# Optimization experiments

Measured on AMD Instinct MI355X. Metric: run time of the kernel, lower is better.

## Reference

```python
import jax, jax.numpy as jnp
import numpy as np

B, S, DIM, H, HD = 4, 1024, 1280, 16, 80
SCALE = HD ** -0.5
ROPE_THETA = 10000.0


def rotate_half(x):
    x1, x2 = jnp.split(x, 2, axis=-1)
    return jnp.concatenate([-x2, x1], axis=-1)


def setup_inputs() -> dict:
    key = jax.random.key(0)
    ks = jax.random.split(key, 5)
    x = jax.random.normal(ks[0], (B, S, DIM), dtype=jnp.float32)
    Wqkv = jax.random.normal(ks[1], (DIM, 3 * DIM), dtype=jnp.float32) * 0.02
    bqkv = jax.random.normal(ks[2], (3 * DIM,), dtype=jnp.float32) * 0.01
    Wproj = jax.random.normal(ks[3], (DIM, DIM), dtype=jnp.float32) * 0.02
    bproj = jax.random.normal(ks[4], (DIM,), dtype=jnp.float32) * 0.01
    # realistic rotary tables: (S, HD) with duplicated freq halves (matches rotate_half layout)
    inv_freq = 1.0 / (ROPE_THETA ** (jnp.arange(0, HD, 2, dtype=jnp.float32) / HD))
    freqs = jnp.outer(jnp.arange(S, dtype=jnp.float32), inv_freq)  # (S, HD/2)
    emb = jnp.concatenate([freqs, freqs], axis=-1)  # (S, HD)
    rope_cos = jnp.cos(emb)
    rope_sin = jnp.sin(emb)
    return {"x": x, "rope_cos": rope_cos, "rope_sin": rope_sin,
            "Wqkv": Wqkv, "bqkv": bqkv, "Wproj": Wproj, "bproj": bproj}


def reference(x, rope_cos, rope_sin, Wqkv, bqkv, Wproj, bproj):
    b, s, d = x.shape
    qkv = (x @ Wqkv + bqkv).reshape(b, s, 3, H, HD)
    q, k, v = qkv[:, :, 0], qkv[:, :, 1], qkv[:, :, 2]  # each (b, s, H, HD)
    cos = rope_cos[None, :, None, :]  # (1, s, 1, HD)
    sin = rope_sin[None, :, None, :]
    q = q * cos + rotate_half(q) * sin
    k = k * cos + rotate_half(k) * sin
    # SDPA with all-ones mask (full attention)
    scores = jnp.einsum("bqhd,bkhd->bhqk", q, k) * SCALE
    probs = jax.nn.softmax(scores, axis=-1)
    out = jnp.einsum("bhqk,bkhd->bqhd", probs, v).reshape(b, s, d)
    return out @ Wproj + bproj
```

## Files before the change

### kernel.cpp

```cpp
#include <hip/hip_runtime.h>
#include <math.h>

#define SCALE_F 0.11180339887498949f
#define HDP 96

typedef short  short8  __attribute__((ext_vector_type(8)));
typedef short  short4v __attribute__((ext_vector_type(4)));
typedef float  f32x4   __attribute__((ext_vector_type(4)));
typedef __bf16 bf16x8  __attribute__((ext_vector_type(8)));

__device__ __forceinline__ float bf2f(short s) {
  union { unsigned u; float f; } v;
  v.u = ((unsigned)(unsigned short)s) << 16;
  return v.f;
}
__device__ __forceinline__ short f2b(float f) {
  __bf16 h = (__bf16)f;
  return __builtin_bit_cast(short, h);
}
__device__ __forceinline__ bool probe_is_bf16(const unsigned* probe) {
  return (probe[1] & 0xFFFFu) != 0u;
}
__device__ __forceinline__ float load_scalar(const void* p, int i, bool isb) {
  return isb ? bf2f(((const short*)p)[i]) : ((const float*)p)[i];
}

__device__ __forceinline__ void gload_lds16(const short* g, short* l) {
  __builtin_amdgcn_global_load_lds(
      (const __attribute__((address_space(1))) void*)g,
      (__attribute__((address_space(3))) void*)l, 16, 0, 0);
}

template <typename V>
__device__ __forceinline__ auto mfma_try(V a, V b, f32x4 c, int)
    -> decltype(__builtin_amdgcn_mfma_f32_16x16x32_bf16(a, b, c, 0, 0, 0)) {
  return __builtin_amdgcn_mfma_f32_16x16x32_bf16(a, b, c, 0, 0, 0);
}
template <typename V>
__device__ __forceinline__ f32x4 mfma_try(V a, V b, f32x4 c, long) {
  return __builtin_amdgcn_mfma_f32_16x16x32_bf16(
      __builtin_bit_cast(bf16x8, a), __builtin_bit_cast(bf16x8, b), c, 0, 0, 0);
}
__device__ __forceinline__ f32x4 MFMA(short8 a, short8 b, f32x4 c) {
  return mfma_try(a, b, c, 0);
}

__global__ __launch_bounds__(256) void cvt_x_kernel(
    const void* __restrict__ xin, short* __restrict__ xout,
    const unsigned* __restrict__ probe) {
  bool isb = probe_is_bf16(probe);
  size_t i = ((size_t)blockIdx.x * 256 + threadIdx.x) * 8;
  if (isb) {
    *(short8*)&xout[i] = *(const short8*)((const short*)xin + i);
  } else {
    const float* f = (const float*)xin + i;
    float4 a0 = *(const float4*)f;
    float4 a1 = *(const float4*)(f + 4);
    short8 sv;
    sv[0] = f2b(a0.x); sv[1] = f2b(a0.y); sv[2] = f2b(a0.z); sv[3] = f2b(a0.w);
    sv[4] = f2b(a1.x); sv[5] = f2b(a1.y); sv[6] = f2b(a1.z); sv[7] = f2b(a1.w);
    *(short8*)&xout[i] = sv;
  }
}

__global__ __launch_bounds__(256) void transpose_kernel(
    const void* __restrict__ in, short* __restrict__ out, int R, int C,
    const unsigned* __restrict__ probe) {
  bool isb = probe_is_bf16(probe);
  __shared__ float tile[32][33];
  int t = threadIdx.x;
  int bx = blockIdx.x;
  int by = blockIdx.y;
  int r = t >> 3, c4 = (t & 7) * 4;
  size_t idx = (size_t)(by * 32 + r) * C + bx * 32 + c4;
  if (isb) {
    short4v v = *(const short4v*)((const short*)in + idx);
    tile[r][c4 + 0] = bf2f(v[0]);
    tile[r][c4 + 1] = bf2f(v[1]);
    tile[r][c4 + 2] = bf2f(v[2]);
    tile[r][c4 + 3] = bf2f(v[3]);
  } else {
    float4 v = *(const float4*)((const float*)in + idx);
    tile[r][c4 + 0] = v.x;
    tile[r][c4 + 1] = v.y;
    tile[r][c4 + 2] = v.z;
    tile[r][c4 + 3] = v.w;
  }
  __syncthreads();
  int rr = t >> 3, k4 = (t & 7) * 4;
  short4v o;
  o[0] = f2b(tile[k4 + 0][rr]);
  o[1] = f2b(tile[k4 + 1][rr]);
  o[2] = f2b(tile[k4 + 2][rr]);
  o[3] = f2b(tile[k4 + 3][rr]);
  *(short4v*)&out[(size_t)(bx * 32 + rr) * R + by * 32 + k4] = o;
}

__global__ __launch_bounds__(512, 2) void gemm_qkv_kernel(
    const short* __restrict__ X, const short* __restrict__ Wt,
    const void* __restrict__ bias, const unsigned* __restrict__ probe,
    short* __restrict__ Qw, short* __restrict__ Kw, short* __restrict__ Vt) {
  const int K = 1280;
  __shared__ short Al[2][2][8192];
  __shared__ short Bl[2][2][8192];
  int t = threadIdx.x;
  int bm = blockIdx.x / 15, bn = blockIdx.x % 15;
  int m0 = bm * 256, n0 = bn * 256;
  int w = t >> 6, lane = t & 63;
  int quad = lane >> 4, l16 = lane & 15, l8 = l16 & 7;
  int arow = (w >> 2) * 64 + l16;
  int brow = (w & 3) * 32 + l16;
  int sr = t >> 3, t8s = t * 8;
  int sjs = (t & 7) ^ (sr & 7);
  int soff0 = ((quad ^ l8) * 8);
  int soff1 = (((4 + quad) ^ l8) * 8);
  f32x4 acc[2][2][4][2] = {};

#define STAGE8(PTR, R0, KOFF, LP)                                            \
  {                                                                          \
    const short* g_ = (PTR) + (size_t)((R0) + sr) * 1280 + (KOFF) + sjs * 8; \
    gload_lds16(g_, (LP) + t8s);                                             \
    gload_lds16(g_ + 64 * 1280, (LP) + t8s + 4096);                          \
  }

#define PHASE(S, HA, HB, QM, QN, STAGE_CODE, DO_VW)                          \
  {                                                                          \
    short8 af[4][2], bfv[2][2];                                              \
    _Pragma("unroll") for (int mt = 0; mt < 4; mt++) {                       \
      int rp_ = (arow + mt * 16) * 64;                                       \
      af[mt][0] = *(const short8*)&Al[S][HA][rp_ + soff0];                   \
      af[mt][1] = *(const short8*)&Al[S][HA][rp_ + soff1];                   \
    }                                                                        \
    _Pragma("unroll") for (int nt = 0; nt < 2; nt++) {                       \
      int rp_ = (brow + nt * 16) * 64;                                       \
      bfv[nt][0] = *(const short8*)&Bl[S][HB][rp_ + soff0];                  \
      bfv[nt][1] = *(const short8*)&Bl[S][HB][rp_ + soff1];                  \
    }                                                                        \
    STAGE_CODE;                                                              \
    __builtin_amdgcn_s_barrier();                                            \
    asm volatile("s_waitcnt lgkmcnt(0)" ::: "memory");                       \
    __builtin_amdgcn_sched_barrier(0);                                       \
    __builtin_amdgcn_s_setprio(1);                                           \
    _Pragma("unroll") for (int mt = 0; mt < 4; mt++)                         \
      _Pragma("unroll") for (int nt = 0; nt < 2; nt++) {                     \
        acc[QM][QN][mt][nt] = MFMA(af[mt][0], bfv[nt][0], acc[QM][QN][mt][nt]); \
        acc[QM][QN][mt][nt] = MFMA(af[mt][1], bfv[nt][1], acc[QM][QN][mt][nt]); \
      }                                                                      \
    __builtin_amdgcn_s_setprio(0);                                           \
    if (DO_VW) {                                                             \
      asm volatile("s_waitcnt vmcnt(4)" ::: "memory");                       \
      __builtin_amdgcn_sched_barrier(0);                                     \
    }                                                                        \
    __builtin_amdgcn_s_barrier();                                            \
  }

  STAGE8(X,  m0,       0,  &Al[0][0][0]);
  STAGE8(X,  m0 + 128, 0,  &Al[0][1][0]);
  STAGE8(Wt, n0,       0,  &Bl[0][0][0]);
  STAGE8(Wt, n0 + 128, 0,  &Bl[0][1][0]);
  STAGE8(X,  m0,       64, &Al[1][0][0]);
  STAGE8(Wt, n0,       64, &Bl[1][0][0]);
  asm volatile("s_waitcnt vmcnt(4)" ::: "memory");
  __builtin_amdgcn_sched_barrier(0);
  __builtin_amdgcn_s_barrier();

  for (int i = 0; i < 10; i++) {
    int k1 = (2 * i + 1) * 64;
    int k2 = (2 * i + 2) * 64; if (k2 >= K) k2 = 0;
    int k3 = (2 * i + 3) * 64; if (k3 >= K) k3 = 0;
    PHASE(0, 0, 0, 0, 0, STAGE8(X,  m0 + 128, k1, &Al[1][1][0]), 0);
    PHASE(0, 0, 1, 0, 1, STAGE8(Wt, n0 + 128, k1, &Bl[1][1][0]), 0);
    PHASE(0, 1, 0, 1, 0, STAGE8(X,  m0,       k2, &Al[0][0][0]), 0);
    PHASE(0, 1, 1, 1, 1, STAGE8(Wt, n0,       k2, &Bl[0][0][0]), 1);
    PHASE(1, 0, 0, 0, 0, STAGE8(X,  m0 + 128, k2, &Al[0][1][0]), 0);
    PHASE(1, 0, 1, 0, 1, STAGE8(Wt, n0 + 128, k2, &Bl[0][1][0]), 0);
    PHASE(1, 1, 0, 1, 0, STAGE8(X,  m0,       k3, &Al[1][0][0]), 0);
    PHASE(1, 1, 1, 1, 1, STAGE8(Wt, n0,       k3, &Bl[1][0][0]), 1);
  }
  asm volatile("s_waitcnt vmcnt(0)" ::: "memory");
  __builtin_amdgcn_sched_barrier(0);

  bool isb = probe_is_bf16(probe);
  float bv[2][2];
#pragma unroll
  for (int qn = 0; qn < 2; qn++)
#pragma unroll
    for (int nt = 0; nt < 2; nt++)
      bv[qn][nt] =
          load_scalar(bias, n0 + qn * 128 + (w & 3) * 32 + nt * 16 + l16, isb);
#pragma unroll
  for (int qm = 0; qm < 2; qm++)
#pragma unroll
    for (int mt = 0; mt < 4; mt++) {
      int mbase = m0 + qm * 128 + (w >> 2) * 64 + mt * 16 + quad * 4;
      int b = mbase >> 10, sbase = mbase & 1023;
#pragma unroll
      for (int qn = 0; qn < 2; qn++)
#pragma unroll
        for (int nt = 0; nt < 2; nt++) {
          int n = n0 + qn * 128 + (w & 3) * 32 + nt * 16 + l16;
          int which = n / 1280;
          int rmod = n - which * 1280;
          int h = rmod / 80;
          int d = rmod - h * 80;
          int bh = b * 16 + h;
          if (which == 2) {
            short4v vv;
#pragma unroll
            for (int reg = 0; reg < 4; reg++)
              vv[reg] = f2b(acc[qm][qn][mt][nt][reg] + bv[qn][nt]);
            *(short4v*)&Vt[((size_t)bh * 80 + d) * 1024 + sbase] = vv;
          } else {
            short* dst = (which == 0 ? Qw : Kw);
#pragma unroll
            for (int reg = 0; reg < 4; reg++)
              dst[((size_t)bh * 1024 + sbase + reg) * HDP + d] =
                  f2b(acc[qm][qn][mt][nt][reg] + bv[qn][nt]);
          }
        }
    }
#undef PHASE
#undef STAGE8
}

__global__ __launch_bounds__(256) void rope_kernel(
    short* __restrict__ Qw, short* __restrict__ Kw,
    const void* __restrict__ cosb, const void* __restrict__ sinb,
    const unsigned* __restrict__ probe) {
  bool isb = probe_is_bf16(probe);
  int t = threadIdx.x;
  int w = t >> 6, lane = t & 63;
  int job = blockIdx.x * 4 + w;
  int which = job & 1;
  int row = job >> 1;
  int s = row & 1023;
  short* ptr = (which ? Kw : Qw) + (size_t)row * HDP;
  float scale = which ? 1.0f : SCALE_F;
  if (lane < 40) {
    float p0 = bf2f(ptr[lane]);
    float p1 = bf2f(ptr[lane + 40]);
    float c0 = load_scalar(cosb, s * 80 + lane, isb);
    float s0 = load_scalar(sinb, s * 80 + lane, isb);
    float c1 = load_scalar(cosb, s * 80 + lane + 40, isb);
    float s1 = load_scalar(sinb, s * 80 + lane + 40, isb);
    ptr[lane] = f2b((p0 * c0 - p1 * s0) * scale);
    ptr[lane + 40] = f2b((p1 * c1 + p0 * s1) * scale);
  } else if (lane < 56) {
    ptr[40 + lane] = 0;
  }
}

__global__ __launch_bounds__(512, 4) void attn_kernel(
    const short* __restrict__ Qw, const short* __restrict__ Kw,
    const short* __restrict__ Vt, short* __restrict__ out) {
  __shared__ short Klds[64 * 104];
  __shared__ short Vlds[80 * 72];
  __shared__ short Ps[8][16 * 72];
  int t = threadIdx.x;
  int w = t >> 6, lane = t & 63;
  int quad = lane >> 4, l16 = lane & 15;
  int bh = blockIdx.x & 63;
  int qt = blockIdx.x >> 6;
  int q0 = qt * 128;
  const short* Kb = Kw + (size_t)bh * 1024 * HDP;
  const short* Vb = Vt + (size_t)bh * 80 * 1024;

  short8 aq[3];
  {
    const short* qrow = Qw + ((size_t)bh * 1024 + q0 + w * 16 + l16) * HDP;
#pragma unroll
    for (int ks = 0; ks < 3; ks++)
      aq[ks] = *(const short8*)&qrow[ks * 32 + quad * 8];
  }

  short8 kreg[2], vreg[2];
#define PREFETCH(c)                                                        \
  {                                                                        \
    {                                                                      \
      int row = t / 12, col = (t % 12) * 8;                                \
      kreg[0] = *(const short8*)&Kb[(size_t)((c) + row) * HDP + col];      \
    }                                                                      \
    if (t < 256) {                                                         \
      int idx = 512 + t;                                                   \
      int row = idx / 12, col = (idx % 12) * 8;                            \
      kreg[1] = *(const short8*)&Kb[(size_t)((c) + row) * HDP + col];      \
    }                                                                      \
    {                                                                      \
      int d = t >> 3, s0 = (t & 7) * 8;                                    \
      vreg[0] = *(const short8*)&Vb[(size_t)d * 1024 + (c) + s0];          \
    }                                                                      \
    if (t < 128) {                                                         \
      int idx = 512 + t;                                                   \
      int d = idx >> 3, s0 = (idx & 7) * 8;                                \
      vreg[1] = *(const short8*)&Vb[(size_t)d * 1024 + (c) + s0];          \
    }                                                                      \
  }
#define STORE_LDS()                                                        \
  {                                                                        \
    {                                                                      \
      int row = t / 12, col = (t % 12) * 8;                                \
      *(short8*)&Klds[row * 104 + col] = kreg[0];                          \
    }                                                                      \
    if (t < 256) {                                                         \
      int idx = 512 + t;                                                   \
      int row = idx / 12, col = (idx % 12) * 8;                            \
      *(short8*)&Klds[row * 104 + col] = kreg[1];                          \
    }                                                                      \
    {                                                                      \
      int d = t >> 3, s0 = (t & 7) * 8;                                    \
      *(short8*)&Vlds[d * 72 + s0] = vreg[0];                              \
    }                                                                      \
    if (t < 128) {                                                         \
      int idx = 512 + t;                                                   \
      int d = idx >> 3, s0 = (idx & 7) * 8;                                \
      *(short8*)&Vlds[d * 72 + s0] = vreg[1];                              \
    }                                                                      \
  }

  PREFETCH(0);
  STORE_LDS();
  __syncthreads();

  f32x4 ofr[5] = {};
  float lsum[4] = {0.f, 0.f, 0.f, 0.f};
  short* Pw = &Ps[w][0];

  for (int c = 0; c < 1024; c += 64) {
    if (c + 64 < 1024) PREFETCH(c + 64);
    f32x4 sf[4] = {};
#pragma unroll
    for (int nt = 0; nt < 4; nt++) {
      short8 bk0 = *(const short8*)&Klds[(nt * 16 + l16) * 104 + 0 * 32 + quad * 8];
      short8 bk1 = *(const short8*)&Klds[(nt * 16 + l16) * 104 + 1 * 32 + quad * 8];
      short8 bk2 = *(const short8*)&Klds[(nt * 16 + l16) * 104 + 2 * 32 + quad * 8];
      sf[nt] = MFMA(aq[0], bk0, sf[nt]);
      sf[nt] = MFMA(aq[1], bk1, sf[nt]);
      sf[nt] = MFMA(aq[2], bk2, sf[nt]);
    }
#pragma unroll
    for (int r = 0; r < 4; r++) {
      float p0 = __expf(fminf(sf[0][r], 30.f));
      float p1 = __expf(fminf(sf[1][r], 30.f));
      float p2 = __expf(fminf(sf[2][r], 30.f));
      float p3 = __expf(fminf(sf[3][r], 30.f));
      sf[0][r] = p0; sf[1][r] = p1; sf[2][r] = p2; sf[3][r] = p3;
      lsum[r] += (p0 + p1) + (p2 + p3);
    }
#pragma unroll
    for (int nt = 0; nt < 4; nt++)
#pragma unroll
      for (int r = 0; r < 4; r++)
        Pw[(quad * 4 + r) * 72 + nt * 16 + l16] = f2b(sf[nt][r]);
    __threadfence_block();
    short8 ap[2];
#pragma unroll
    for (int ks = 0; ks < 2; ks++)
      ap[ks] = *(const short8*)&Pw[l16 * 72 + ks * 32 + quad * 8];
#pragma unroll
    for (int nt = 0; nt < 5; nt++) {
      short8 bv0 = *(const short8*)&Vlds[(nt * 16 + l16) * 72 + 0 * 32 + quad * 8];
      short8 bv1 = *(const short8*)&Vlds[(nt * 16 + l16) * 72 + 1 * 32 + quad * 8];
      ofr[nt] = MFMA(ap[0], bv0, ofr[nt]);
      ofr[nt] = MFMA(ap[1], bv1, ofr[nt]);
    }
    __syncthreads();
    if (c + 64 < 1024) {
      STORE_LDS();
      __syncthreads();
    }
  }
#pragma unroll
  for (int off = 1; off < 16; off <<= 1)
#pragma unroll
    for (int r = 0; r < 4; r++) lsum[r] += __shfl_xor(lsum[r], off);
  float inv[4];
#pragma unroll
  for (int r = 0; r < 4; r++) inv[r] = 1.f / lsum[r];
  int b = bh >> 4, h = bh & 15;
#pragma unroll
  for (int nt = 0; nt < 5; nt++) {
    int d = nt * 16 + l16;
#pragma unroll
    for (int r = 0; r < 4; r++) {
      int s = q0 + w * 16 + quad * 4 + r;
      out[((size_t)(b * 1024 + s)) * 1280 + h * 80 + d] = f2b(ofr[nt][r] * inv[r]);
    }
  }
}

__global__ __launch_bounds__(256) void gemm_proj_kernel(
    const short* __restrict__ A, const short* __restrict__ Wt,
    const void* __restrict__ bias, const unsigned* __restrict__ probe,
    float* __restrict__ out) {
  const int K = 1280;
  __shared__ short As[2][128 * 32];
  __shared__ short Bs[2][128 * 32];
  int t = threadIdx.x;
  int bm = blockIdx.x / 10;
  int bn = blockIdx.x % 10;
  int m0 = bm * 128, n0 = bn * 128;
  int w = t >> 6, lane = t & 63;
  int wm = w & 1, wn = w >> 1;
  int quad = lane >> 4, l16 = lane & 15;
  int row = t >> 2, ch = (t & 3) * 8, row2 = row + 64;
  int t8 = t * 8;
  const short* Ar  = A  + (size_t)(m0 + row)  * K + ch;
  const short* Ar2 = A  + (size_t)(m0 + row2) * K + ch;
  const short* Wr  = Wt + (size_t)(n0 + row)  * K + ch;
  const short* Wr2 = Wt + (size_t)(n0 + row2) * K + ch;
  f32x4 acc[4][4] = {};
  gload_lds16(Ar,  &As[0][t8]);
  gload_lds16(Ar2, &As[0][t8 + 2048]);
  gload_lds16(Wr,  &Bs[0][t8]);
  gload_lds16(Wr2, &Bs[0][t8 + 2048]);
  __syncthreads();
  int p = 0;
#define PROJ_COMPUTE(pp)                                                      \
  {                                                                           \
    short8 af[4], bfr[4];                                                     \
    _Pragma("unroll") for (int mt = 0; mt < 4; mt++)                          \
        af[mt] = *(const short8*)&As[pp][(wm * 64 + mt * 16 + l16) * 32 + quad * 8]; \
    _Pragma("unroll") for (int nt = 0; nt < 4; nt++)                          \
        bfr[nt] = *(const short8*)&Bs[pp][(wn * 64 + nt * 16 + l16) * 32 + quad * 8]; \
    _Pragma("unroll") for (int mt = 0; mt < 4; mt++)                          \
        _Pragma("unroll") for (int nt = 0; nt < 4; nt++)                      \
            acc[mt][nt] = MFMA(af[mt], bfr[nt], acc[mt][nt]);                 \
  }
  for (int k0 = 32; k0 < K; k0 += 32, p ^= 1) {
    gload_lds16(Ar + k0,  &As[p ^ 1][t8]);
    gload_lds16(Ar2 + k0, &As[p ^ 1][t8 + 2048]);
    gload_lds16(Wr + k0,  &Bs[p ^ 1][t8]);
    gload_lds16(Wr2 + k0, &Bs[p ^ 1][t8 + 2048]);
    PROJ_COMPUTE(p);
    __syncthreads();
  }
  PROJ_COMPUTE(p);
  bool isb = probe_is_bf16(probe);
  float bv[4];
#pragma unroll
  for (int nt = 0; nt < 4; nt++)
    bv[nt] = load_scalar(bias, n0 + wn * 64 + nt * 16 + l16, isb);
#pragma unroll
  for (int mt = 0; mt < 4; mt++) {
#pragma unroll
    for (int nt = 0; nt < 4; nt++) {
      int n = n0 + wn * 64 + nt * 16 + l16;
#pragma unroll
      for (int reg = 0; reg < 4; reg++) {
        int m = m0 + wm * 64 + mt * 16 + quad * 4 + reg;
        out[(size_t)m * 1280 + n] = acc[mt][nt][reg] + bv[nt];
      }
    }
  }
}

extern "C" void kernel_launch(void* const* d_in, const int* in_sizes, int n_in,
                              void* d_out, int out_size, void* d_ws, size_t ws_size,
                              hipStream_t stream) {
  const void* x        = d_in[0];
  const void* rope_cos = d_in[1];
  const void* rope_sin = d_in[2];
  const void* Wqkv     = d_in[3];
  const void* bqkv     = d_in[4];
  const void* Wproj    = d_in[5];
  const void* bproj    = d_in[6];
  const unsigned* probe = (const unsigned*)rope_cos;
  char* ws = (char*)d_ws;
  short* Wt1 = (short*)(ws + 0);
  short* Wt2 = (short*)(ws + 9830400);
  short* Qw  = (short*)(ws + 13107200);
  short* Kw  = (short*)(ws + 25690112);
  short* Vt  = (short*)(ws + 38273024);
  short* Xb  = (short*)(ws + 48758784);
  short* At  = (short*)(ws + 48758784);

  cvt_x_kernel<<<2560, 256, 0, stream>>>(x, Xb, probe);
  transpose_kernel<<<dim3(3840 / 32, 1280 / 32), 256, 0, stream>>>(Wqkv, Wt1, 1280, 3840, probe);
  transpose_kernel<<<dim3(1280 / 32, 1280 / 32), 256, 0, stream>>>(Wproj, Wt2, 1280, 1280, probe);
  gemm_qkv_kernel<<<240, 512, 0, stream>>>(Xb, Wt1, bqkv, probe, Qw, Kw, Vt);
  rope_kernel<<<32768, 256, 0, stream>>>(Qw, Kw, rope_cos, rope_sin, probe);
  attn_kernel<<<512, 512, 0, stream>>>(Qw, Kw, Vt, At);
  gemm_proj_kernel<<<32 * 10, 256, 0, stream>>>(At, Wt2, bproj, probe, (float*)d_out);
}
```

Measured before the change: 244.4 us.

## Double-buffer attention K/V tiles in LDS and drop redundant barriers

The attention kernel now keeps two LDS buffers for the K and V tiles, alternating between them each iteration. The next tile is stored into the buffer not being read, which removes one __syncthreads per key chunk. Separately, the GEMM phase macro drops the s_barrier that sat between staging and the MFMA block, leaving only the trailing barrier. The double buffer roughly doubles the K/V LDS footprint, which may lower how many attention blocks fit per CU. The removed GEMM barrier relies on the remaining barriers and waitcnts to keep LDS reads and writes correctly ordered.

```diff
diff --git a/kernel.cpp b/kernel.cpp
--- a/kernel.cpp
+++ b/kernel.cpp
@@ -137,7 +137,6 @@
       bfv[nt][1] = *(const short8*)&Bl[S][HB][rp_ + soff1];                  \
     }                                                                        \
     STAGE_CODE;                                                              \
-    __builtin_amdgcn_s_barrier();                                            \
     asm volatile("s_waitcnt lgkmcnt(0)" ::: "memory");                       \
     __builtin_amdgcn_sched_barrier(0);                                       \
     __builtin_amdgcn_s_setprio(1);                                           \
@@ -253,8 +252,8 @@
 __global__ __launch_bounds__(512, 4) void attn_kernel(
     const short* __restrict__ Qw, const short* __restrict__ Kw,
     const short* __restrict__ Vt, short* __restrict__ out) {
-  __shared__ short Klds[64 * 104];
-  __shared__ short Vlds[80 * 72];
+  __shared__ short Klds[2][64 * 104];
+  __shared__ short Vlds[2][80 * 72];
   __shared__ short Ps[8][16 * 72];
   int t = threadIdx.x;
   int w = t >> 6, lane = t & 63;
@@ -295,44 +294,47 @@
       vreg[1] = *(const short8*)&Vb[(size_t)d * 1024 + (c) + s0];          \
     }                                                                      \
   }
-#define STORE_LDS()                                                        \
+#define STORE_LDS(P)                                                       \
   {                                                                        \
     {                                                                      \
       int row = t / 12, col = (t % 12) * 8;                                \
-      *(short8*)&Klds[row * 104 + col] = kreg[0];                          \
+      *(short8*)&Klds[P][row * 104 + col] = kreg[0];                       \
     }                                                                      \
     if (t < 256) {                                                         \
       int idx = 512 + t;                                                   \
       int row = idx / 12, col = (idx % 12) * 8;                            \
-      *(short8*)&Klds[row * 104 + col] = kreg[1];                          \
+      *(short8*)&Klds[P][row * 104 + col] = kreg[1];                       \
     }                                                                      \
     {                                                                      \
       int d = t >> 3, s0 = (t & 7) * 8;                                    \
-      *(short8*)&Vlds[d * 72 + s0] = vreg[0];                              \
+      *(short8*)&Vlds[P][d * 72 + s0] = vreg[0];                           \
     }                                                                      \
     if (t < 128) {                                                         \
       int idx = 512 + t;                                                   \
       int d = idx >> 3, s0 = (idx & 7) * 8;                                \
-      *(short8*)&Vlds[d * 72 + s0] = vreg[1];                              \
+      *(short8*)&Vlds[P][d * 72 + s0] = vreg[1];                           \
     }                                                                      \
   }
 
   PREFETCH(0);
-  STORE_LDS();
+  STORE_LDS(0);
   __syncthreads();
 
   f32x4 ofr[5] = {};
   float lsum[4] = {0.f, 0.f, 0.f, 0.f};
   short* Pw = &Ps[w][0];
 
-  for (int c = 0; c < 1024; c += 64) {
+  int p = 0;
+  for (int c = 0; c < 1024; c += 64, p ^= 1) {
     if (c + 64 < 1024) PREFETCH(c + 64);
+    const short* Kl = &Klds[p][0];
+    const short* Vl = &Vlds[p][0];
     f32x4 sf[4] = {};
 #pragma unroll
     for (int nt = 0; nt < 4; nt++) {
-      short8 bk0 = *(const short8*)&Klds[(nt * 16 + l16) * 104 + 0 * 32 + quad * 8];
-      short8 bk1 = *(const short8*)&Klds[(nt * 16 + l16) * 104 + 1 * 32 + quad * 8];
-      short8 bk2 = *(const short8*)&Klds[(nt * 16 + l16) * 104 + 2 * 32 + quad * 8];
+      short8 bk0 = *(const short8*)&Kl[(nt * 16 + l16) * 104 + 0 * 32 + quad * 8];
+      short8 bk1 = *(const short8*)&Kl[(nt * 16 + l16) * 104 + 1 * 32 + quad * 8];
+      short8 bk2 = *(const short8*)&Kl[(nt * 16 + l16) * 104 + 2 * 32 + quad * 8];
       sf[nt] = MFMA(aq[0], bk0, sf[nt]);
       sf[nt] = MFMA(aq[1], bk1, sf[nt]);
       sf[nt] = MFMA(aq[2], bk2, sf[nt]);
@@ -358,14 +360,13 @@
       ap[ks] = *(const short8*)&Pw[l16 * 72 + ks * 32 + quad * 8];
 #pragma unroll
     for (int nt = 0; nt < 5; nt++) {
-      short8 bv0 = *(const short8*)&Vlds[(nt * 16 + l16) * 72 + 0 * 32 + quad * 8];
-      short8 bv1 = *(const short8*)&Vlds[(nt * 16 + l16) * 72 + 1 * 32 + quad * 8];
+      short8 bv0 = *(const short8*)&Vl[(nt * 16 + l16) * 72 + 0 * 32 + quad * 8];
+      short8 bv1 = *(const short8*)&Vl[(nt * 16 + l16) * 72 + 1 * 32 + quad * 8];
       ofr[nt] = MFMA(ap[0], bv0, ofr[nt]);
       ofr[nt] = MFMA(ap[1], bv1, ofr[nt]);
     }
-    __syncthreads();
     if (c + 64 < 1024) {
-      STORE_LDS();
+      STORE_LDS(p ^ 1);
       __syncthreads();
     }
   }
```

After: 242.7 us. About the same (-0.7%).
